# Kernel optimization log

Hardware: AMD Instinct MI355X
Metric: run time of the kernel (lower is better)

The kernel has to match this reference:

```python
import jax, jax.numpy as jnp
import numpy as np

B, S, IN_DIM, CTX = 32, 512, 256, 128
D, H, L = 128, 4, 2
DH = D // H
HID = 512
TOTAL = 11 * D * D + 8 * D  # hypernet flat weight size per sample
EPS = 1e-5


def _layernorm(x, g, b):
    mu = jnp.mean(x, axis=-1, keepdims=True)
    var = jnp.mean(jnp.square(x - mu), axis=-1, keepdims=True)
    return (x - mu) * jax.lax.rsqrt(var + EPS) * g + b


def setup_inputs() -> dict:
    key = jax.random.key(0)
    ks = jax.random.split(key, 24)
    f32 = jnp.float32
    inp = {
        'x': jax.random.normal(ks[0], (B, S, IN_DIM), f32),
        'context_vector': jax.random.normal(ks[1], (B, CTX), f32),
        'in_proj_w': jax.random.normal(ks[2], (D, IN_DIM), f32) * (IN_DIM ** -0.5),
        'in_proj_b': jnp.zeros((D,), f32),
        'pe': jax.random.normal(ks[3], (1, S, D), f32) * 0.02,
        'hfc1_w': jax.random.normal(ks[4], (L, HID, CTX), f32) * (CTX ** -0.5),
        'hfc1_b': jnp.zeros((L, HID), f32),
        'hfc2_w': jax.random.normal(ks[5], (L, TOTAL, HID), f32) * 0.02,
        'hfc2_b': jnp.zeros((L, TOTAL), f32),
        'out_proj_w': jax.random.normal(ks[6], (L, D, D), f32) * (D ** -0.5),
        'out_proj_b': jnp.zeros((L, D), f32),
        'ln1_g': jnp.ones((L, D), f32), 'ln1_b': jnp.zeros((L, D), f32),
        'ln2_g': jnp.ones((L, D), f32), 'ln2_b': jnp.zeros((L, D), f32),
        'alpha1': jnp.full((L,), 0.5, f32), 'alpha2': jnp.full((L,), 0.5, f32),
        'head_w': jax.random.normal(ks[7], (1, D), f32) * (D ** -0.5),
        'head_b': jnp.zeros((1,), f32),
    }
    return inp


def reference(x, context_vector, in_proj_w, in_proj_b, pe, hfc1_w, hfc1_b,
              hfc2_w, hfc2_b, out_proj_w, out_proj_b, ln1_g, ln1_b,
              ln2_g, ln2_b, alpha1, alpha2, head_w, head_b):
    # input projection + learned positional encoding
    h = jnp.einsum('bsi,di->bsd', x, in_proj_w) + in_proj_b
    h = h + pe[:, :h.shape[1], :]

    # flat split offsets for hypernet output
    sizes = [3 * D * D, 3 * D, 4 * D * D, 4 * D, 4 * D * D, D]
    offs = np.concatenate([[0], np.cumsum(sizes)])

    for l in range(L):
        # hypernet: per-sample weights from context
        hid = jax.nn.relu(context_vector @ hfc1_w[l].T + hfc1_b[l])
        flat = hid @ hfc2_w[l].T + hfc2_b[l]  # [B, TOTAL]
        aw = flat[:, offs[0]:offs[1]].reshape(B, 3 * D, D)
        ab = flat[:, offs[1]:offs[2]]                     # [B, 3D]
        f1w = flat[:, offs[2]:offs[3]].reshape(B, 4 * D, D)
        f1b = flat[:, offs[3]:offs[4]]                    # [B, 4D]
        f2w = flat[:, offs[4]:offs[5]].reshape(B, D, 4 * D)
        f2b = flat[:, offs[5]:offs[6]]                    # [B, D]

        # per-sample QKV projection (grouped GEMM over batch)
        qkv = jnp.einsum('bsd,bed->bse', h, aw) + ab[:, None, :]
        q, k, v = jnp.split(qkv, 3, axis=-1)
        q = q.reshape(B, S, H, DH)
        k = k.reshape(B, S, H, DH)
        v = v.reshape(B, S, H, DH)
        scores = jnp.einsum('bqhd,bkhd->bhqk', q, k) / jnp.sqrt(jnp.float32(DH))
        attn = jax.nn.softmax(scores, axis=-1)
        ctx = jnp.einsum('bhqk,bkhd->bqhd', attn, v).reshape(B, S, D)
        attn_out = jnp.einsum('bsd,ed->bse', ctx, out_proj_w[l]) + out_proj_b[l]

        h = _layernorm(h + alpha1[l] * attn_out, ln1_g[l], ln1_b[l])

        # per-sample FFN
        ff = jax.nn.relu(jnp.einsum('bsd,bfd->bsf', h, f1w) + f1b[:, None, :])
        ff = jnp.einsum('bsf,bdf->bsd', ff, f2w) + f2b[:, None, :]

        h = _layernorm(h + alpha2[l] * ff, ln2_g[l], ln2_b[l])

    out = h[:, -1, :] @ head_w.T + head_b  # [B, 1]
    return out
```

## Files before the change

### kernel.cpp

```cpp
#include <hip/hip_runtime.h>
#include <hip/hip_bf16.h>

constexpr int B_    = 32;
constexpr int S_    = 512;
constexpr int INDIM = 256;
constexpr int KCTX  = 128;
constexpr int D_    = 128;
constexpr int H_    = 4;
constexpr int L_    = 2;
constexpr int HID_  = 512;
constexpr int TOTAL_ = 11 * D_ * D_ + 8 * D_;
constexpr int OFF_AB  = 3 * D_ * D_;
constexpr int OFF_F1W = OFF_AB + 3 * D_;
constexpr int OFF_F1B = OFF_F1W + 4 * D_ * D_;
constexpr int OFF_F2W = OFF_F1B + 4 * D_;
constexpr int OFF_F2B = OFF_F2W + 4 * D_ * D_;
constexpr int TP = 132;

typedef __attribute__((ext_vector_type(8))) short short8;
typedef __attribute__((ext_vector_type(4))) short short4v;
typedef __attribute__((ext_vector_type(2))) short short2v;
typedef __attribute__((ext_vector_type(4))) float f32x4;

#define MFMA16 __builtin_amdgcn_mfma_f32_16x16x32_bf16

__device__ __forceinline__ short f2bf(float f) {
  __hip_bfloat16 h = __float2bfloat16(f);
  return __builtin_bit_cast(short, h);
}
__device__ __forceinline__ float bf2f(short s) {
  __hip_bfloat16 h = __builtin_bit_cast(__hip_bfloat16, s);
  return __bfloat162float(h);
}
struct bfpair { short hi, lo; };
__device__ __forceinline__ bfpair split2p(float x) {
  bfpair p;
  p.hi = f2bf(x);
  p.lo = f2bf(x - bf2f(p.hi));
  return p;
}

__device__ __forceinline__ long ftaddr(int row, int k, int K) {
  return ((long)(row >> 4) * (K >> 3) + (k >> 3)) * 128 + (row & 15) * 8 + (k & 7);
}

__global__ void k_cvtft(const float* __restrict__ in, short* __restrict__ oh,
                        short* __restrict__ ol, int ktShift, int n8) {
  int t = blockIdx.x * 256 + threadIdx.x;
  if (t >= n8) return;
  int kt = 1 << ktShift;
  int row = t >> ktShift;
  int kc = t & (kt - 1);
  const float* p = in + ((long)row << (ktShift + 3)) + kc * 8;
  float4 v0 = *(const float4*)p;
  float4 v1 = *(const float4*)(p + 4);
  short8 h8, l8;
  bfpair q;
  q = split2p(v0.x); h8[0] = q.hi; l8[0] = q.lo;
  q = split2p(v0.y); h8[1] = q.hi; l8[1] = q.lo;
  q = split2p(v0.z); h8[2] = q.hi; l8[2] = q.lo;
  q = split2p(v0.w); h8[3] = q.hi; l8[3] = q.lo;
  q = split2p(v1.x); h8[4] = q.hi; l8[4] = q.lo;
  q = split2p(v1.y); h8[5] = q.hi; l8[5] = q.lo;
  q = split2p(v1.z); h8[6] = q.hi; l8[6] = q.lo;
  q = split2p(v1.w); h8[7] = q.hi; l8[7] = q.lo;
  long o = ((long)(row >> 4) * kt + kc) * 128 + (row & 15) * 8;
  *(short8*)(oh + o) = h8;
  *(short8*)(ol + o) = l8;
}

__global__ __launch_bounds__(512) void k_hid(const float* __restrict__ cvec,
                                             const float* __restrict__ w,
                                             const float* __restrict__ bias,
                                             short* __restrict__ hh,
                                             short* __restrict__ hl) {
  int lb = blockIdx.x;
  int b  = lb & 31;
  int j  = threadIdx.x;
  __shared__ float cs[KCTX];
  if (j < KCTX) cs[j] = cvec[b * KCTX + j];
  __syncthreads();
  int l = lb >> 5;
  const float* wr = w + (long)(l * HID_ + j) * KCTX;
  float s = bias[l * HID_ + j];
  #pragma unroll
  for (int c = 0; c < KCTX; c += 4) {
    float4 cv = *(const float4*)(cs + c);
    float4 wv = *(const float4*)(wr + c);
    s += cv.x * wv.x + cv.y * wv.y + cv.z * wv.z + cv.w * wv.w;
  }
  s = fmaxf(s, 0.f);
  bfpair p = split2p(s);
  long o = (long)l * 32 * HID_ + ((long)(b >> 4) * 64 + (j >> 3)) * 128 + (b & 15) * 8 + (j & 7);
  hh[o] = p.hi;
  hl[o] = p.lo;
}

__global__ __launch_bounds__(256) void k_flat(
    const short* __restrict__ hidh, const short* __restrict__ hidl,
    const float* __restrict__ W, const float* __restrict__ bias,
    short* __restrict__ awh, short* __restrict__ awl,
    short* __restrict__ f1h, short* __restrict__ f1l,
    short* __restrict__ f2h, short* __restrict__ f2l,
    float* __restrict__ ab, float* __restrict__ f1b, float* __restrict__ f2b) {
  __shared__ short wls[2][64 * 64];
  const int l = blockIdx.y;
  hidh += (long)l * 32 * HID_;
  hidl += (long)l * 32 * HID_;
  W    += (long)l * TOTAL_ * HID_;
  bias += (long)l * TOTAL_;
  awh  += (long)l * B_ * 49152;  awl += (long)l * B_ * 49152;
  f1h  += (long)l * B_ * 65536;  f1l += (long)l * B_ * 65536;
  f2h  += (long)l * B_ * 65536;  f2l += (long)l * B_ * 65536;
  ab   += l * B_ * 384;  f1b += l * B_ * 512;  f2b += l * B_ * 128;
  const int tid = threadIdx.x, wave = tid >> 6, lane = tid & 63;
  const int r = lane & 15, g = lane >> 4;
  const int nb0 = blockIdx.x * 64;
  const int rr = tid >> 4;
  const int cc = (tid & 15) * 4;
  const float* wbase = W + (long)nb0 * HID_;
  float4 wv[2][4];
  #pragma unroll
  for (int rnd = 0; rnd < 4; ++rnd) {
    wv[0][rnd] = *(const float4*)(wbase + (long)(rnd * 16 + rr) * HID_ + cc);
    wv[1][rnd] = *(const float4*)(wbase + (long)(rnd * 16 + rr) * HID_ + 64 + cc);
  }
  const short* pAh = hidh + g * 128 + r * 8;
  const short* pAl = hidl + g * 128 + r * 8;
  f32x4 acc0 = {0, 0, 0, 0}, acc1 = {0, 0, 0, 0};
  int cur = 0;
  for (int c0 = 0; c0 < 512; c0 += 64) {
    #pragma unroll
    for (int rnd = 0; rnd < 4; ++rnd) {
      int row = rnd * 16 + rr;
      short4v h4, l4; bfpair q;
      q = split2p(wv[cur][rnd].x); h4[0] = q.hi; l4[0] = q.lo;
      q = split2p(wv[cur][rnd].y); h4[1] = q.hi; l4[1] = q.lo;
      q = split2p(wv[cur][rnd].z); h4[2] = q.hi; l4[2] = q.lo;
      q = split2p(wv[cur][rnd].w); h4[3] = q.hi; l4[3] = q.lo;
      int sb = row * 128 + ((cc * 2) ^ ((row & 7) << 4));
      *(short4v*)((char*)&wls[0][0] + sb) = h4;
      *(short4v*)((char*)&wls[1][0] + sb) = l4;
    }
    if (c0 + 128 < 512) {
      #pragma unroll
      for (int rnd = 0; rnd < 4; ++rnd)
        wv[cur][rnd] = *(const float4*)(wbase + (long)(rnd * 16 + rr) * HID_ + (c0 + 128) + cc);
    }
    __syncthreads();
    #pragma unroll
    for (int kk = 0; kk < 2; ++kk) {
      long ao = (long)(c0 * 16) + kk * 512;
      short8 ah0 = *(const short8*)(pAh + ao);
      short8 ah1 = *(const short8*)(pAh + 8192 + ao);
      short8 al0 = *(const short8*)(pAl + ao);
      short8 al1 = *(const short8*)(pAl + 8192 + ao);
      int wrow = wave * 16 + r;
      int wb = wrow * 128 + ((kk * 64 + g * 16) ^ ((r & 7) << 4));
      short8 wh = *(const short8*)((char*)&wls[0][0] + wb);
      short8 wl = *(const short8*)((char*)&wls[1][0] + wb);
      acc0 = MFMA16(ah0, wl, acc0, 0, 0, 0);
      acc0 = MFMA16(al0, wh, acc0, 0, 0, 0);
      acc0 = MFMA16(ah0, wh, acc0, 0, 0, 0);
      acc1 = MFMA16(ah1, wl, acc1, 0, 0, 0);
      acc1 = MFMA16(al1, wh, acc1, 0, 0, 0);
      acc1 = MFMA16(ah1, wh, acc1, 0, 0, 0);
    }
    __syncthreads();
    cur ^= 1;
  }
  constexpr int TPF = 68;
  float* tile = (float*)&wls[0][0];
  {
    int trow = nb0 + wave * 16 + r;
    float bv = bias[trow];
    int col = wave * 16 + r;
    #pragma unroll
    for (int reg = 0; reg < 4; ++reg) {
      tile[(g * 4 + reg) * TPF + col]        = acc0[reg] + bv;
      tile[(g * 4 + reg + 16) * TPF + col]   = acc1[reg] + bv;
    }
  }
  __syncthreads();
  {
    int b  = tid >> 3;
    int cg = tid & 7;
    int t0 = nb0 + cg * 8;
    float v[8];
    #pragma unroll
    for (int j = 0; j < 8; ++j) v[j] = tile[b * TPF + cg * 8 + j];
    if (t0 < OFF_AB) {
      int e = t0 >> 7, d = t0 & 127;
      long a = (long)b * 49152 + ((long)(e >> 4) * 16 + (d >> 3)) * 128 + (e & 15) * 8;
      short8 h8, l8; bfpair q;
      #pragma unroll
      for (int j = 0; j < 8; ++j) { q = split2p(v[j]); h8[j] = q.hi; l8[j] = q.lo; }
      *(short8*)(awh + a) = h8;
      *(short8*)(awl + a) = l8;
    } else if (t0 < OFF_F1W) {
      float* dst = ab + b * 384 + (t0 - OFF_AB);
      float4 x0 = {v[0], v[1], v[2], v[3]}, x1 = {v[4], v[5], v[6], v[7]};
      *(float4*)dst = x0; *(float4*)(dst + 4) = x1;
    } else if (t0 < OFF_F1B) {
      int i = t0 - OFF_F1W; int f = i >> 7, d = i & 127;
      long a = (long)b * 65536 + ((long)(f >> 4) * 16 + (d >> 3)) * 128 + (f & 15) * 8;
      short8 h8, l8; bfpair q;
      #pragma unroll
      for (int j = 0; j < 8; ++j) { q = split2p(v[j]); h8[j] = q.hi; l8[j] = q.lo; }
      *(short8*)(f1h + a) = h8;
      *(short8*)(f1l + a) = l8;
    } else if (t0 < OFF_F2W) {
      float* dst = f1b + b * 512 + (t0 - OFF_F1B);
      float4 x0 = {v[0], v[1], v[2], v[3]}, x1 = {v[4], v[5], v[6], v[7]};
      *(float4*)dst = x0; *(float4*)(dst + 4) = x1;
    } else if (t0 < OFF_F2B) {
      int i = t0 - OFF_F2W; int dd = i >> 9, f = i & 511;
      long a = (long)b * 65536 + ((long)(dd >> 4) * 64 + (f >> 3)) * 128 + (dd & 15) * 8;
      short8 h8, l8; bfpair q;
      #pragma unroll
      for (int j = 0; j < 8; ++j) { q = split2p(v[j]); h8[j] = q.hi; l8[j] = q.lo; }
      *(short8*)(f2h + a) = h8;
      *(short8*)(f2l + a) = l8;
    } else {
      float* dst = f2b + b * 128 + (t0 - OFF_F2B);
      float4 x0 = {v[0], v[1], v[2], v[3]}, x1 = {v[4], v[5], v[6], v[7]};
      *(float4*)dst = x0; *(float4*)(dst + 4) = x1;
    }
  }
}

template <int K, int EPI, bool RELU>
__global__ __launch_bounds__(256) void k_gemm(
    const short* __restrict__ Ah, const short* __restrict__ Al, long sA,
    const short* __restrict__ Wh, const short* __restrict__ Wl, long sW,
    const float* __restrict__ biasP, long sB,
    void* __restrict__ p0, void* __restrict__ p1,
    void* __restrict__ p2, void* __restrict__ p3,
    const float* __restrict__ pe, int N,
    const float* __restrict__ lng, const float* __restrict__ lnb,
    const float* __restrict__ lnal, int mOff, int nOff) {
  extern __shared__ char smem_dyn[];
  const int tid = threadIdx.x, wave = tid >> 6, lane = tid & 63;
  const int r = lane & 15, g = lane >> 4;
  const int b = blockIdx.z;
  const int bx = blockIdx.x + mOff, by = blockIdx.y + nOff;
  const int m0 = bx * 64 + (wave & 1) * 32;
  const int n0 = by * 128 + (wave >> 1) * 64;
  const long KT = (long)K * 16;
  const short* pAh = Ah + (long)b * sA + (m0 >> 4) * KT + g * 128 + r * 8;
  const short* pAl = Al + (long)b * sA + (m0 >> 4) * KT + g * 128 + r * 8;
  const short* pWh = Wh + (long)b * sW + (n0 >> 4) * KT + g * 128 + r * 8;
  const short* pWl = Wl + (long)b * sW + (n0 >> 4) * KT + g * 128 + r * 8;
  f32x4 acc[2][4] = {{{0,0,0,0},{0,0,0,0},{0,0,0,0},{0,0,0,0}},
                     {{0,0,0,0},{0,0,0,0},{0,0,0,0},{0,0,0,0}}};
  for (int kk = 0; kk < K / 32; ++kk) {
    long ko = (long)kk * 512;
    short8 a0h = *(const short8*)(pAh + ko);
    short8 a1h = *(const short8*)(pAh + KT + ko);
    short8 a0l = *(const short8*)(pAl + ko);
    short8 a1l = *(const short8*)(pAl + KT + ko);
    #pragma unroll
    for (int ns = 0; ns < 4; ++ns) {
      short8 wh = *(const short8*)(pWh + ns * KT + ko);
      short8 wl = *(const short8*)(pWl + ns * KT + ko);
      acc[0][ns] = MFMA16(a0h, wl, acc[0][ns], 0, 0, 0);
      acc[0][ns] = MFMA16(a0l, wh, acc[0][ns], 0, 0, 0);
      acc[0][ns] = MFMA16(a0h, wh, acc[0][ns], 0, 0, 0);
      acc[1][ns] = MFMA16(a1h, wl, acc[1][ns], 0, 0, 0);
      acc[1][ns] = MFMA16(a1l, wh, acc[1][ns], 0, 0, 0);
      acc[1][ns] = MFMA16(a1h, wh, acc[1][ns], 0, 0, 0);
    }
  }

  if constexpr (EPI == 5) {
    if (by == 2) {
      #pragma unroll
      for (int ms = 0; ms < 2; ++ms) {
        int crow0 = m0 + ms * 16 + g * 4;
        #pragma unroll
        for (int ns = 0; ns < 4; ++ns) {
          int ccol = n0 + ns * 16 + r;
          float bv = biasP[(long)b * sB + ccol];
          int c2 = ccol - 256, hd = c2 >> 5, dd = c2 & 31;
          short4v h4, l4; bfpair q;
          #pragma unroll
          for (int reg = 0; reg < 4; ++reg) {
            float v = acc[ms][ns][reg] + bv;
            q = split2p(v); h4[reg] = q.hi; l4[reg] = q.lo;
          }
          long o = (long)(b * 4 + hd) * 16384 + (dd >> 4) * 8192
                 + (crow0 >> 3) * 128 + (dd & 15) * 8 + (crow0 & 7);
          *(short4v*)((short*)p2 + o) = h4;
          *(short4v*)((short*)p3 + o) = l4;
        }
      }
      return;
    }
  }

  if constexpr (EPI == 1) {
    #pragma unroll
    for (int ms = 0; ms < 2; ++ms) {
      #pragma unroll
      for (int ns = 0; ns < 4; ++ns) {
        int ccol = n0 + ns * 16 + r;
        float bv = biasP[ccol];
        #pragma unroll
        for (int reg = 0; reg < 4; ++reg) {
          int crow = m0 + ms * 16 + g * 4 + reg;
          float v = acc[ms][ns][reg] + bv + pe[crow * D_ + ccol];
          ((float*)p0)[((long)b * S_ + crow) * D_ + ccol] = v;
          long o = (long)b * 65536 + (long)(crow >> 4) * 2048
                 + (ccol >> 3) * 128 + (crow & 15) * 8 + (ccol & 7);
          bfpair sp = split2p(v);
          ((short*)p1)[o] = sp.hi;
          ((short*)p2)[o] = sp.lo;
        }
      }
    }
    return;
  }

  float* tile = (float*)smem_dyn;
  #pragma unroll
  for (int ms = 0; ms < 2; ++ms) {
    #pragma unroll
    for (int ns = 0; ns < 4; ++ns) {
      int ccol = n0 + ns * 16 + r;
      float bv = biasP[(long)b * sB + ccol];
      #pragma unroll
      for (int reg = 0; reg < 4; ++reg) {
        float v = acc[ms][ns][reg] + bv;
        if constexpr (RELU) v = fmaxf(v, 0.f);
        int trow2 = (wave & 1) * 32 + ms * 16 + g * 4 + reg;
        int tcol = (wave >> 1) * 64 + ns * 16 + r;
        tile[trow2 * TP + tcol] = v;
      }
    }
  }
  __syncthreads();

  if constexpr (EPI == 0 || EPI == 5) {
    int row = tid >> 2, cg = tid & 3;
    int crow = bx * 64 + row;
    long rowbase = (long)b * 512 * N + (long)(crow >> 4) * (16 * (long)N) + (crow & 15) * 8;
    #pragma unroll
    for (int j4 = 0; j4 < 4; ++j4) {
      int tcol = j4 * 32 + cg * 8;
      float4 aa = *(const float4*)&tile[row * TP + tcol];
      float4 bb = *(const float4*)&tile[row * TP + tcol + 4];
      short8 h8, l8; bfpair q;
      q = split2p(aa.x); h8[0] = q.hi; l8[0] = q.lo;
      q = split2p(aa.y); h8[1] = q.hi; l8[1] = q.lo;
      q = split2p(aa.z); h8[2] = q.hi; l8[2] = q.lo;
      q = split2p(aa.w); h8[3] = q.hi; l8[3] = q.lo;
      q = split2p(bb.x); h8[4] = q.hi; l8[4] = q.lo;
      q = split2p(bb.y); h8[5] = q.hi; l8[5] = q.lo;
      q = split2p(bb.z); h8[6] = q.hi; l8[6] = q.lo;
      q = split2p(bb.w); h8[7] = q.hi; l8[7] = q.lo;
      int ccol = by * 128 + tcol;
      long o = rowbase + (long)(ccol >> 3) * 128;
      *(short8*)((short*)p0 + o) = h8;
      *(short8*)((short*)p1 + o) = l8;
    }
  } else if constexpr (EPI == 4) {
    int row = tid >> 2, q = tid & 3;
    int brow = bx * 64 + row;
    float a = lnal[0];
    float* hf = (float*)p0;
    float* hrow = hf + ((long)b * S_ + brow) * D_ + q * 32;
    float tv[32];
    float s = 0.f, ss = 0.f;
    #pragma unroll
    for (int i = 0; i < 32; i += 4) {
      float4 hv = *(const float4*)(hrow + i);
      float4 yv = *(const float4*)&tile[row * TP + q * 32 + i];
      float t0 = hv.x + a * yv.x, t1 = hv.y + a * yv.y;
      float t2 = hv.z + a * yv.z, t3 = hv.w + a * yv.w;
      tv[i] = t0; tv[i+1] = t1; tv[i+2] = t2; tv[i+3] = t3;
      s += t0 + t1 + t2 + t3;
      ss += t0*t0 + t1*t1 + t2*t2 + t3*t3;
    }
    s  += __shfl_xor(s, 1);  s  += __shfl_xor(s, 2);
    ss += __shfl_xor(ss, 1); ss += __shfl_xor(ss, 2);
    float mu = s * (1.f / 128.f);
    float varv = ss * (1.f / 128.f) - mu * mu;
    float inv = rsqrtf(varv + 1e-5f);
    short* ph = (short*)p1; short* pl = (short*)p2;
    long fb = (long)b * 65536 + (long)(brow >> 4) * 2048 + (brow & 15) * 8;
    #pragma unroll
    for (int j = 0; j < 4; ++j) {
      short8 hv8, lv8;
      #pragma unroll
      for (int e = 0; e < 8; e += 4) {
        int i = j * 8 + e;
        int c = q * 32 + i;
        float4 gv = *(const float4*)(lng + c);
        float4 bb = *(const float4*)(lnb + c);
        float4 o4;
        o4.x = (tv[i]   - mu) * inv * gv.x + bb.x;
        o4.y = (tv[i+1] - mu) * inv * gv.y + bb.y;
        o4.z = (tv[i+2] - mu) * inv * gv.z + bb.z;
        o4.w = (tv[i+3] - mu) * inv * gv.w + bb.w;
        *(float4*)(hrow + i) = o4;
        bfpair q0 = split2p(o4.x); hv8[e]   = q0.hi; lv8[e]   = q0.lo;
        bfpair q1 = split2p(o4.y); hv8[e+1] = q1.hi; lv8[e+1] = q1.lo;
        bfpair q2 = split2p(o4.z); hv8[e+2] = q2.hi; lv8[e+2] = q2.lo;
        bfpair q3 = split2p(o4.w); hv8[e+3] = q3.hi; lv8[e+3] = q3.lo;
      }
      long o = fb + (q * 4 + j) * 128;
      *(short8*)(ph + o) = hv8;
      *(short8*)(pl + o) = lv8;
    }
  }
}

__global__ __launch_bounds__(128) void k_attn(const short* __restrict__ qkh,
                                              const short* __restrict__ qkl,
                                              const short* __restrict__ vth,
                                              const short* __restrict__ vtl,
                                              short* __restrict__ ch,
                                              short* __restrict__ cl,
                                              int mOff) {
  __shared__ __align__(16) float scr[16][516];
  __shared__ __align__(16) float obuf[16][34];
  const int tid = threadIdx.x, wave = tid >> 6, lane = tid & 63;
  const int r = lane & 15, g = lane >> 4;
  const int b = blockIdx.z, hh = blockIdx.y;
  const int m0 = (blockIdx.x + mOff) * 16;
  const long qb = (long)b * 131072;
  const long qoff = qb + (long)(m0 >> 4) * 4096 + (hh * 4 + g) * 128 + r * 8;
  short8 qh = *(const short8*)(qkh + qoff);
  short8 ql = *(const short8*)(qkl + qoff);
  const float sc = 0.17677669529663687f;
  for (int n0 = wave * 256; n0 < wave * 256 + 256; n0 += 16) {
    long koff = qb + (long)(n0 >> 4) * 4096 + (16 + hh * 4 + g) * 128 + r * 8;
    short8 kh = *(const short8*)(qkh + koff);
    short8 kl = *(const short8*)(qkl + koff);
    f32x4 s = {0, 0, 0, 0};
    s = MFMA16(qh, kl, s, 0, 0, 0);
    s = MFMA16(ql, kh, s, 0, 0, 0);
    s = MFMA16(qh, kh, s, 0, 0, 0);
    #pragma unroll
    for (int reg = 0; reg < 4; ++reg)
      scr[g * 4 + reg][n0 + r] = s[reg] * sc;
  }
  __syncthreads();
  for (int row = wave * 8; row < wave * 8 + 8; ++row) {
    float v[8];
    #pragma unroll
    for (int i = 0; i < 8; ++i) v[i] = scr[row][lane + i * 64];
    float m = v[0];
    #pragma unroll
    for (int i = 1; i < 8; ++i) m = fmaxf(m, v[i]);
    #pragma unroll
    for (int o = 32; o > 0; o >>= 1) m = fmaxf(m, __shfl_xor(m, o));
    float ssum = 0.f;
    #pragma unroll
    for (int i = 0; i < 8; ++i) { v[i] = __expf(v[i] - m); ssum += v[i]; }
    #pragma unroll
    for (int o = 32; o > 0; o >>= 1) ssum += __shfl_xor(ssum, o);
    float inv = 1.f / ssum;
    #pragma unroll
    for (int i = 0; i < 8; ++i) scr[row][lane + i * 64] = v[i] * inv;
  }
  __syncthreads();
  f32x4 o0 = {0, 0, 0, 0}, o1 = {0, 0, 0, 0};
  const long vb = (long)(b * 4 + hh) * 16384;
  for (int kt = wave * 8; kt < wave * 8 + 8; ++kt) {
    float4 pv0 = *(const float4*)&scr[r][kt * 32 + g * 8];
    float4 pv1 = *(const float4*)&scr[r][kt * 32 + g * 8 + 4];
    short8 pah, pal;
    bfpair p;
    p = split2p(pv0.x); pah[0] = p.hi; pal[0] = p.lo;
    p = split2p(pv0.y); pah[1] = p.hi; pal[1] = p.lo;
    p = split2p(pv0.z); pah[2] = p.hi; pal[2] = p.lo;
    p = split2p(pv0.w); pah[3] = p.hi; pal[3] = p.lo;
    p = split2p(pv1.x); pah[4] = p.hi; pal[4] = p.lo;
    p = split2p(pv1.y); pah[5] = p.hi; pal[5] = p.lo;
    p = split2p(pv1.z); pah[6] = p.hi; pal[6] = p.lo;
    p = split2p(pv1.w); pah[7] = p.hi; pal[7] = p.lo;
    long vo = vb + (long)(kt * 4 + g) * 128 + r * 8;
    short8 vh0 = *(const short8*)(vth + vo);
    short8 vh1 = *(const short8*)(vth + vo + 8192);
    short8 vl0 = *(const short8*)(vtl + vo);
    short8 vl1 = *(const short8*)(vtl + vo + 8192);
    o0 = MFMA16(pah, vl0, o0, 0, 0, 0);
    o0 = MFMA16(pal, vh0, o0, 0, 0, 0);
    o0 = MFMA16(pah, vh0, o0, 0, 0, 0);
    o1 = MFMA16(pah, vl1, o1, 0, 0, 0);
    o1 = MFMA16(pal, vh1, o1, 0, 0, 0);
    o1 = MFMA16(pah, vh1, o1, 0, 0, 0);
  }
  if (wave == 1) {
    #pragma unroll
    for (int reg = 0; reg < 4; ++reg) {
      obuf[g * 4 + reg][r] = o0[reg];
      obuf[g * 4 + reg][17 + r] = o1[reg];
    }
  }
  __syncthreads();
  if (wave == 0) {
    #pragma unroll
    for (int reg = 0; reg < 4; ++reg) {
      float a0 = o0[reg] + obuf[g * 4 + reg][r];
      float a1 = o1[reg] + obuf[g * 4 + reg][17 + r];
      int srow = m0 + g * 4 + reg;
      int col0 = hh * 32 + r;
      long o = (long)b * 65536 + (long)(srow >> 4) * 2048
             + (col0 >> 3) * 128 + (srow & 15) * 8 + (col0 & 7);
      bfpair sp0 = split2p(a0);
      ch[o] = sp0.hi; cl[o] = sp0.lo;
      long o2 = o + 2 * 128;
      bfpair sp1 = split2p(a1);
      ch[o2] = sp1.hi; cl[o2] = sp1.lo;
    }
  }
}

__global__ __launch_bounds__(64) void k_head(const float* __restrict__ h,
                                             const float* __restrict__ hw,
                                             const float* __restrict__ hb,
                                             float* __restrict__ out) {
  int b = blockIdx.x, lane = threadIdx.x;
  const float* hr = h + ((long)b * S_ + (S_ - 1)) * D_;
  float v = hr[lane] * hw[lane] + hr[lane + 64] * hw[lane + 64];
  #pragma unroll
  for (int o = 32; o > 0; o >>= 1) v += __shfl_xor(v, o);
  if (lane == 0) out[b] = v + hb[0];
}

extern "C" void kernel_launch(void* const* d_in, const int* in_sizes, int n_in,
                              void* d_out, int out_size, void* d_ws, size_t ws_size,
                              hipStream_t stream) {
  const float* x    = (const float*)d_in[0];
  const float* cvec = (const float*)d_in[1];
  const float* ipw  = (const float*)d_in[2];
  const float* ipb  = (const float*)d_in[3];
  const float* pe   = (const float*)d_in[4];
  const float* h1w  = (const float*)d_in[5];
  const float* h1b  = (const float*)d_in[6];
  const float* h2w  = (const float*)d_in[7];
  const float* h2b  = (const float*)d_in[8];
  const float* opw  = (const float*)d_in[9];
  const float* opb  = (const float*)d_in[10];
  const float* ln1g = (const float*)d_in[11];
  const float* ln1b = (const float*)d_in[12];
  const float* ln2g = (const float*)d_in[13];
  const float* ln2b = (const float*)d_in[14];
  const float* a1   = (const float*)d_in[15];
  const float* a2   = (const float*)d_in[16];
  const float* hw   = (const float*)d_in[17];
  const float* hb   = (const float*)d_in[18];
  float* out = (float*)d_out;

  char* ws = (char*)d_ws;
  size_t off = 0;
  auto alloc = [&](size_t n) { void* p = ws + off; off = (off + n + 255) & ~(size_t)255; return p; };

  const long AWs = (long)B_ * 49152;
  const long F1s = (long)B_ * 65536;
  const long F2s = (long)B_ * 65536;

  short* ff1h  = (short*)alloc((size_t)B_ * S_ * 512 * 2);
  short* ff1l  = (short*)alloc((size_t)B_ * S_ * 512 * 2);
  short* xFh   = ff1h;
  short* xFl   = ff1l;
  float* h_f   = (float*)alloc((size_t)B_ * S_ * D_ * 4);
  short* hFh   = (short*)alloc((size_t)B_ * S_ * D_ * 2);
  short* hFl   = (short*)alloc((size_t)B_ * S_ * D_ * 2);
  short* hidFh = (short*)alloc((size_t)L_ * 32 * HID_ * 2);
  short* hidFl = (short*)alloc((size_t)L_ * 32 * HID_ * 2);
  short* awFh  = (short*)alloc((size_t)L_ * AWs * 2);
  short* awFl  = (short*)alloc((size_t)L_ * AWs * 2);
  short* f1wFh = (short*)alloc((size_t)L_ * F1s * 2);
  short* f1wFl = (short*)alloc((size_t)L_ * F1s * 2);
  short* f2wFh = (short*)alloc((size_t)L_ * F2s * 2);
  short* f2wFl = (short*)alloc((size_t)L_ * F2s * 2);
  float* abF   = (float*)alloc((size_t)L_ * B_ * 384 * 4);
  float* f1bF  = (float*)alloc((size_t)L_ * B_ * 512 * 4);
  float* f2bF  = (float*)alloc((size_t)L_ * B_ * 128 * 4);
  short* qkFh  = (short*)alloc((size_t)B_ * S_ * 256 * 2);
  short* qkFl  = (short*)alloc((size_t)B_ * S_ * 256 * 2);
  short* vtFh  = (short*)alloc((size_t)B_ * H_ * 32 * S_ * 2);
  short* vtFl  = (short*)alloc((size_t)B_ * H_ * 32 * S_ * 2);
  short* cxFh  = (short*)alloc((size_t)B_ * S_ * D_ * 2);
  short* cxFl  = (short*)alloc((size_t)B_ * S_ * D_ * 2);
  short* ipwFh = (short*)alloc((size_t)D_ * INDIM * 2);
  short* ipwFl = (short*)alloc((size_t)D_ * INDIM * 2);
  short* opwFh = (short*)alloc((size_t)L_ * D_ * D_ * 2);
  short* opwFl = (short*)alloc((size_t)L_ * D_ * D_ * 2);

  k_cvtft<<<(B_ * S_ * INDIM / 8 + 255) / 256, 256, 0, stream>>>(x, xFh, xFl, 5, B_ * S_ * INDIM / 8);
  k_cvtft<<<16, 256, 0, stream>>>(ipw, ipwFh, ipwFl, 5, D_ * INDIM / 8);
  k_cvtft<<<16, 256, 0, stream>>>(opw, opwFh, opwFl, 4, L_ * D_ * D_ / 8);

  k_hid<<<L_ * 32, 512, 0, stream>>>(cvec, h1w, h1b, hidFh, hidFl);

  k_flat<<<dim3(TOTAL_ / 64, 2), 256, 0, stream>>>(
      hidFh, hidFl, h2w, h2b, awFh, awFl, f1wFh, f1wFl, f2wFh, f2wFl,
      abF, f1bF, f2bF);

  k_gemm<INDIM, 1, false><<<dim3(8, 1, B_), 256, 0, stream>>>(
      xFh, xFl, (long)S_ * INDIM, ipwFh, ipwFl, 0, ipb, 0,
      h_f, hFh, hFl, nullptr, pe, 128, nullptr, nullptr, nullptr, 0, 0);

  constexpr size_t TILE_LDS = 64 * TP * 4;

  {
    int l = 0;
    k_gemm<D_, 5, false><<<dim3(8, 3, B_), 256, TILE_LDS, stream>>>(
        hFh, hFl, (long)S_ * D_, awFh + l * AWs, awFl + l * AWs, 49152,
        abF + l * B_ * 384, 384,
        qkFh, qkFl, vtFh, vtFl, nullptr, 256, nullptr, nullptr, nullptr, 0, 0);
    k_attn<<<dim3(S_ / 16, H_, B_), 128, 0, stream>>>(qkFh, qkFl, vtFh, vtFl, cxFh, cxFl, 0);
    k_gemm<D_, 4, false><<<dim3(8, 1, B_), 256, TILE_LDS, stream>>>(
        cxFh, cxFl, (long)S_ * D_, opwFh + l * 16384, opwFl + l * 16384, 0,
        opb + l * D_, 0, h_f, hFh, hFl, nullptr, nullptr, 128,
        ln1g + l * D_, ln1b + l * D_, a1 + l, 0, 0);
    k_gemm<D_, 0, true><<<dim3(8, 4, B_), 256, TILE_LDS, stream>>>(
        hFh, hFl, (long)S_ * D_, f1wFh + l * F1s, f1wFl + l * F1s, 65536,
        f1bF + l * B_ * 512, 512,
        ff1h, ff1l, nullptr, nullptr, nullptr, 512, nullptr, nullptr, nullptr, 0, 0);
    k_gemm<512, 4, false><<<dim3(8, 1, B_), 256, TILE_LDS, stream>>>(
        ff1h, ff1l, (long)S_ * 512, f2wFh + l * F2s, f2wFl + l * F2s, 65536,
        f2bF + l * B_ * 128, 128,
        h_f, hFh, hFl, nullptr, nullptr, 128,
        ln2g + l * D_, ln2b + l * D_, a2 + l, 0, 0);
  }

  {
    int l = 1;
    k_gemm<D_, 5, false><<<dim3(8, 2, B_), 256, TILE_LDS, stream>>>(
        hFh, hFl, (long)S_ * D_, awFh + l * AWs, awFl + l * AWs, 49152,
        abF + l * B_ * 384, 384,
        qkFh, qkFl, vtFh, vtFl, nullptr, 256, nullptr, nullptr, nullptr, 0, 1);
    k_gemm<D_, 5, false><<<dim3(1, 1, B_), 256, TILE_LDS, stream>>>(
        hFh, hFl, (long)S_ * D_, awFh + l * AWs, awFl + l * AWs, 49152,
        abF + l * B_ * 384, 384,
        qkFh, qkFl, vtFh, vtFl, nullptr, 256, nullptr, nullptr, nullptr, 7, 0);
    k_attn<<<dim3(1, H_, B_), 128, 0, stream>>>(qkFh, qkFl, vtFh, vtFl, cxFh, cxFl, 31);
    k_gemm<D_, 4, false><<<dim3(1, 1, B_), 256, TILE_LDS, stream>>>(
        cxFh, cxFl, (long)S_ * D_, opwFh + l * 16384, opwFl + l * 16384, 0,
        opb + l * D_, 0, h_f, hFh, hFl, nullptr, nullptr, 128,
        ln1g + l * D_, ln1b + l * D_, a1 + l, 7, 0);
    k_gemm<D_, 0, true><<<dim3(1, 4, B_), 256, TILE_LDS, stream>>>(
        hFh, hFl, (long)S_ * D_, f1wFh + l * F1s, f1wFl + l * F1s, 65536,
        f1bF + l * B_ * 512, 512,
        ff1h, ff1l, nullptr, nullptr, nullptr, 512, nullptr, nullptr, nullptr, 7, 0);
    k_gemm<512, 4, false><<<dim3(1, 1, B_), 256, TILE_LDS, stream>>>(
        ff1h, ff1l, (long)S_ * 512, f2wFh + l * F2s, f2wFl + l * F2s, 65536,
        f2bF + l * B_ * 128, 128,
        h_f, hFh, hFl, nullptr, nullptr, 128,
        ln2g + l * D_, ln2b + l * D_, a2 + l, 7, 0);
  }
  k_head<<<B_, 64, 0, stream>>>(h_f, hw, hb, out);
}
```

Measured before the change: 448.3 us.

## Merge prep kernels, co-schedule input projection with hypernet GEMM, fuse layer-1 QKV launches

Three conversion kernels and the hypernet hidden-layer kernel are folded into one launch that dispatches on block id. The input projection GEMM now runs as extra blocks inside the hypernet flat-weight kernel, so the two independent GEMMs share one launch and fill the GPU together. The two layer-1 QKV launches are merged into one grid through a block remapping mode. The aim is fewer launches and less idle time in small grids, at the cost of more branching and possible register or LDS pressure in the combined kernels.

New measurement: 440.2 us. Within noise of the previous version (-1.8%).

```diff
diff --git a/kernel.cpp b/kernel.cpp
--- a/kernel.cpp
+++ b/kernel.cpp
@@ -40,13 +40,10 @@
   return p;
 }
 
-__device__ __forceinline__ long ftaddr(int row, int k, int K) {
-  return ((long)(row >> 4) * (K >> 3) + (k >> 3)) * 128 + (row & 15) * 8 + (k & 7);
-}
-
-__global__ void k_cvtft(const float* __restrict__ in, short* __restrict__ oh,
-                        short* __restrict__ ol, int ktShift, int n8) {
-  int t = blockIdx.x * 256 + threadIdx.x;
+__device__ __forceinline__ void cvt_body(const float* __restrict__ in,
+                                         short* __restrict__ oh,
+                                         short* __restrict__ ol,
+                                         int ktShift, int n8, int t) {
   if (t >= n8) return;
   int kt = 1 << ktShift;
   int row = t >> ktShift;
@@ -54,8 +51,7 @@
   const float* p = in + ((long)row << (ktShift + 3)) + kc * 8;
   float4 v0 = *(const float4*)p;
   float4 v1 = *(const float4*)(p + 4);
-  short8 h8, l8;
-  bfpair q;
+  short8 h8, l8; bfpair q;
   q = split2p(v0.x); h8[0] = q.hi; l8[0] = q.lo;
   q = split2p(v0.y); h8[1] = q.hi; l8[1] = q.lo;
   q = split2p(v0.z); h8[2] = q.hi; l8[2] = q.lo;
@@ -69,42 +65,125 @@
   *(short8*)(ol + o) = l8;
 }
 
-__global__ __launch_bounds__(512) void k_hid(const float* __restrict__ cvec,
-                                             const float* __restrict__ w,
-                                             const float* __restrict__ bias,
-                                             short* __restrict__ hh,
-                                             short* __restrict__ hl) {
-  int lb = blockIdx.x;
-  int b  = lb & 31;
-  int j  = threadIdx.x;
-  __shared__ float cs[KCTX];
-  if (j < KCTX) cs[j] = cvec[b * KCTX + j];
-  __syncthreads();
-  int l = lb >> 5;
-  const float* wr = w + (long)(l * HID_ + j) * KCTX;
-  float s = bias[l * HID_ + j];
+__global__ __launch_bounds__(256) void k_prep(
+    const float* __restrict__ x, const float* __restrict__ ipw,
+    const float* __restrict__ opw,
+    short* __restrict__ xFh, short* __restrict__ xFl,
+    short* __restrict__ ipwFh, short* __restrict__ ipwFl,
+    short* __restrict__ opwFh, short* __restrict__ opwFl,
+    const float* __restrict__ cvec, const float* __restrict__ h1w,
+    const float* __restrict__ h1b,
+    short* __restrict__ hidFh, short* __restrict__ hidFl) {
+  int id = blockIdx.x, tid = threadIdx.x;
+  if (id < 2048) {
+    cvt_body(x, xFh, xFl, 5, B_ * S_ * INDIM / 8, id * 256 + tid);
+  } else if (id < 2064) {
+    cvt_body(ipw, ipwFh, ipwFl, 5, D_ * INDIM / 8, (id - 2048) * 256 + tid);
+  } else if (id < 2080) {
+    cvt_body(opw, opwFh, opwFl, 4, L_ * D_ * D_ / 8, (id - 2064) * 256 + tid);
+  } else {
+    int hb = id - 2080;
+    int l = hb >> 5, b = hb & 31;
+    __shared__ float cs[KCTX];
+    if (tid < KCTX) cs[tid] = cvec[b * KCTX + tid];
+    __syncthreads();
+    #pragma unroll
+    for (int jj = 0; jj < 2; ++jj) {
+      int j = tid + jj * 256;
+      const float* wr = h1w + (long)(l * HID_ + j) * KCTX;
+      float s = h1b[l * HID_ + j];
+      #pragma unroll
+      for (int c = 0; c < KCTX; c += 4) {
+        float4 cv = *(const float4*)(cs + c);
+        float4 wv = *(const float4*)(wr + c);
+        s += cv.x * wv.x + cv.y * wv.y + cv.z * wv.z + cv.w * wv.w;
+      }
+      s = fmaxf(s, 0.f);
+      bfpair p = split2p(s);
+      long o = (long)l * 32 * HID_ + ((long)(b >> 4) * 64 + (j >> 3)) * 128
+             + (b & 15) * 8 + (j & 7);
+      hidFh[o] = p.hi;
+      hidFl[o] = p.lo;
+    }
+  }
+}
+
+__device__ void inproj_block(int id,
+    const short* __restrict__ xFh, const short* __restrict__ xFl,
+    const short* __restrict__ ipwFh, const short* __restrict__ ipwFl,
+    const float* __restrict__ ipb, const float* __restrict__ pe,
+    float* __restrict__ h_f, short* __restrict__ hFh, short* __restrict__ hFl) {
+  const int tid = threadIdx.x, wave = tid >> 6, lane = tid & 63;
+  const int r = lane & 15, g = lane >> 4;
+  const int bx = id >> 5, b = id & 31;
+  const int m0 = bx * 64 + (wave & 1) * 32;
+  const int n0 = (wave >> 1) * 64;
+  const long KT = (long)INDIM * 16;
+  const short* pAh = xFh + (long)b * S_ * INDIM + (m0 >> 4) * KT + g * 128 + r * 8;
+  const short* pAl = xFl + (long)b * S_ * INDIM + (m0 >> 4) * KT + g * 128 + r * 8;
+  const short* pWh = ipwFh + (n0 >> 4) * KT + g * 128 + r * 8;
+  const short* pWl = ipwFl + (n0 >> 4) * KT + g * 128 + r * 8;
+  f32x4 acc[2][4] = {{{0,0,0,0},{0,0,0,0},{0,0,0,0},{0,0,0,0}},
+                     {{0,0,0,0},{0,0,0,0},{0,0,0,0},{0,0,0,0}}};
+  for (int kk = 0; kk < INDIM / 32; ++kk) {
+    long ko = (long)kk * 512;
+    short8 a0h = *(const short8*)(pAh + ko);
+    short8 a1h = *(const short8*)(pAh + KT + ko);
+    short8 a0l = *(const short8*)(pAl + ko);
+    short8 a1l = *(const short8*)(pAl + KT + ko);
+    #pragma unroll
+    for (int ns = 0; ns < 4; ++ns) {
+      short8 wh = *(const short8*)(pWh + ns * KT + ko);
+      short8 wl = *(const short8*)(pWl + ns * KT + ko);
+      acc[0][ns] = MFMA16(a0h, wl, acc[0][ns], 0, 0, 0);
+      acc[0][ns] = MFMA16(a0l, wh, acc[0][ns], 0, 0, 0);
+      acc[0][ns] = MFMA16(a0h, wh, acc[0][ns], 0, 0, 0);
+      acc[1][ns] = MFMA16(a1h, wl, acc[1][ns], 0, 0, 0);
+      acc[1][ns] = MFMA16(a1l, wh, acc[1][ns], 0, 0, 0);
+      acc[1][ns] = MFMA16(a1h, wh, acc[1][ns], 0, 0, 0);
+    }
+  }
   #pragma unroll
-  for (int c = 0; c < KCTX; c += 4) {
-    float4 cv = *(const float4*)(cs + c);
-    float4 wv = *(const float4*)(wr + c);
-    s += cv.x * wv.x + cv.y * wv.y + cv.z * wv.z + cv.w * wv.w;
-  }
-  s = fmaxf(s, 0.f);
-  bfpair p = split2p(s);
-  long o = (long)l * 32 * HID_ + ((long)(b >> 4) * 64 + (j >> 3)) * 128 + (b & 15) * 8 + (j & 7);
-  hh[o] = p.hi;
-  hl[o] = p.lo;
-}
-
-__global__ __launch_bounds__(256) void k_flat(
+  for (int ms = 0; ms < 2; ++ms) {
+    #pragma unroll
+    for (int ns = 0; ns < 4; ++ns) {
+      int ccol = n0 + ns * 16 + r;
+      float bv = ipb[ccol];
+      #pragma unroll
+      for (int reg = 0; reg < 4; ++reg) {
+        int crow = m0 + ms * 16 + g * 4 + reg;
+        float v = acc[ms][ns][reg] + bv + pe[crow * D_ + ccol];
+        h_f[((long)b * S_ + crow) * D_ + ccol] = v;
+        long o = (long)b * 65536 + (long)(crow >> 4) * 2048
+               + (ccol >> 3) * 128 + (crow & 15) * 8 + (ccol & 7);
+        bfpair sp = split2p(v);
+        hFh[o] = sp.hi;
+        hFl[o] = sp.lo;
+      }
+    }
+  }
+}
+
+__global__ __launch_bounds__(256) void k_flat_ip(
     const short* __restrict__ hidh, const short* __restrict__ hidl,
     const float* __restrict__ W, const float* __restrict__ bias,
     short* __restrict__ awh, short* __restrict__ awl,
     short* __restrict__ f1h, short* __restrict__ f1l,
     short* __restrict__ f2h, short* __restrict__ f2l,
-    float* __restrict__ ab, float* __restrict__ f1b, float* __restrict__ f2b) {
+    float* __restrict__ ab, float* __restrict__ f1b, float* __restrict__ f2b,
+    const short* __restrict__ xFh, const short* __restrict__ xFl,
+    const short* __restrict__ ipwFh, const short* __restrict__ ipwFl,
+    const float* __restrict__ ipb, const float* __restrict__ pe,
+    float* __restrict__ h_f, short* __restrict__ hFh, short* __restrict__ hFl) {
   __shared__ short wls[2][64 * 64];
-  const int l = blockIdx.y;
+  const int id = blockIdx.x;
+  if (id < 256) {
+    inproj_block(id, xFh, xFl, ipwFh, ipwFl, ipb, pe, h_f, hFh, hFl);
+    return;
+  }
+  const int fid = id - 256;
+  const int l = fid / 2832;
+  const int bxf = fid % 2832;
   hidh += (long)l * 32 * HID_;
   hidl += (long)l * 32 * HID_;
   W    += (long)l * TOTAL_ * HID_;
@@ -115,7 +194,7 @@
   ab   += l * B_ * 384;  f1b += l * B_ * 512;  f2b += l * B_ * 128;
   const int tid = threadIdx.x, wave = tid >> 6, lane = tid & 63;
   const int r = lane & 15, g = lane >> 4;
-  const int nb0 = blockIdx.x * 64;
+  const int nb0 = bxf * 64;
   const int rr = tid >> 4;
   const int cc = (tid & 15) * 4;
   const float* wbase = W + (long)nb0 * HID_;
@@ -172,13 +251,12 @@
   constexpr int TPF = 68;
   float* tile = (float*)&wls[0][0];
   {
-    int trow = nb0 + wave * 16 + r;
-    float bv = bias[trow];
+    float bv = bias[nb0 + wave * 16 + r];
     int col = wave * 16 + r;
     #pragma unroll
     for (int reg = 0; reg < 4; ++reg) {
-      tile[(g * 4 + reg) * TPF + col]        = acc0[reg] + bv;
-      tile[(g * 4 + reg + 16) * TPF + col]   = acc1[reg] + bv;
+      tile[(g * 4 + reg) * TPF + col]      = acc0[reg] + bv;
+      tile[(g * 4 + reg + 16) * TPF + col] = acc1[reg] + bv;
     }
   }
   __syncthreads();
@@ -236,14 +314,21 @@
     const float* __restrict__ biasP, long sB,
     void* __restrict__ p0, void* __restrict__ p1,
     void* __restrict__ p2, void* __restrict__ p3,
-    const float* __restrict__ pe, int N,
+    int N,
     const float* __restrict__ lng, const float* __restrict__ lnb,
-    const float* __restrict__ lnal, int mOff, int nOff) {
+    const float* __restrict__ lnal, int mOff, int nOff, int mode) {
   extern __shared__ char smem_dyn[];
   const int tid = threadIdx.x, wave = tid >> 6, lane = tid & 63;
   const int r = lane & 15, g = lane >> 4;
   const int b = blockIdx.z;
-  const int bx = blockIdx.x + mOff, by = blockIdx.y + nOff;
+  int bx, by;
+  if (mode == 1) {
+    int xx = blockIdx.x;
+    if (xx < 16) { bx = xx >> 1; by = 1 + (xx & 1); }
+    else         { bx = 7; by = 0; }
+  } else {
+    bx = blockIdx.x + mOff; by = blockIdx.y + nOff;
+  }
   const int m0 = bx * 64 + (wave & 1) * 32;
   const int n0 = by * 128 + (wave >> 1) * 64;
   const long KT = (long)K * 16;
@@ -296,29 +381,6 @@
       }
       return;
     }
-  }
-
-  if constexpr (EPI == 1) {
-    #pragma unroll
-    for (int ms = 0; ms < 2; ++ms) {
-      #pragma unroll
-      for (int ns = 0; ns < 4; ++ns) {
-        int ccol = n0 + ns * 16 + r;
-        float bv = biasP[ccol];
-        #pragma unroll
-        for (int reg = 0; reg < 4; ++reg) {
-          int crow = m0 + ms * 16 + g * 4 + reg;
-          float v = acc[ms][ns][reg] + bv + pe[crow * D_ + ccol];
-          ((float*)p0)[((long)b * S_ + crow) * D_ + ccol] = v;
-          long o = (long)b * 65536 + (long)(crow >> 4) * 2048
-                 + (ccol >> 3) * 128 + (crow & 15) * 8 + (ccol & 7);
-          bfpair sp = split2p(v);
-          ((short*)p1)[o] = sp.hi;
-          ((short*)p2)[o] = sp.lo;
-        }
-      }
-    }
-    return;
   }
 
   float* tile = (float*)smem_dyn;
@@ -591,19 +653,13 @@
   short* opwFh = (short*)alloc((size_t)L_ * D_ * D_ * 2);
   short* opwFl = (short*)alloc((size_t)L_ * D_ * D_ * 2);
 
-  k_cvtft<<<(B_ * S_ * INDIM / 8 + 255) / 256, 256, 0, stream>>>(x, xFh, xFl, 5, B_ * S_ * INDIM / 8);
-  k_cvtft<<<16, 256, 0, stream>>>(ipw, ipwFh, ipwFl, 5, D_ * INDIM / 8);
-  k_cvtft<<<16, 256, 0, stream>>>(opw, opwFh, opwFl, 4, L_ * D_ * D_ / 8);
-
-  k_hid<<<L_ * 32, 512, 0, stream>>>(cvec, h1w, h1b, hidFh, hidFl);
-
-  k_flat<<<dim3(TOTAL_ / 64, 2), 256, 0, stream>>>(
+  k_prep<<<2144, 256, 0, stream>>>(x, ipw, opw, xFh, xFl, ipwFh, ipwFl,
+                                   opwFh, opwFl, cvec, h1w, h1b, hidFh, hidFl);
+
+  k_flat_ip<<<256 + 2 * 2832, 256, 0, stream>>>(
       hidFh, hidFl, h2w, h2b, awFh, awFl, f1wFh, f1wFl, f2wFh, f2wFl,
-      abF, f1bF, f2bF);
-
-  k_gemm<INDIM, 1, false><<<dim3(8, 1, B_), 256, 0, stream>>>(
-      xFh, xFl, (long)S_ * INDIM, ipwFh, ipwFl, 0, ipb, 0,
-      h_f, hFh, hFl, nullptr, pe, 128, nullptr, nullptr, nullptr, 0, 0);
+      abF, f1bF, f2bF,
+      xFh, xFl, ipwFh, ipwFl, ipb, pe, h_f, hFh, hFl);
 
   constexpr size_t TILE_LDS = 64 * TP * 4;
 
@@ -612,47 +668,43 @@
     k_gemm<D_, 5, false><<<dim3(8, 3, B_), 256, TILE_LDS, stream>>>(
         hFh, hFl, (long)S_ * D_, awFh + l * AWs, awFl + l * AWs, 49152,
         abF + l * B_ * 384, 384,
-        qkFh, qkFl, vtFh, vtFl, nullptr, 256, nullptr, nullptr, nullptr, 0, 0);
+        qkFh, qkFl, vtFh, vtFl, 256, nullptr, nullptr, nullptr, 0, 0, 0);
     k_attn<<<dim3(S_ / 16, H_, B_), 128, 0, stream>>>(qkFh, qkFl, vtFh, vtFl, cxFh, cxFl, 0);
     k_gemm<D_, 4, false><<<dim3(8, 1, B_), 256, TILE_LDS, stream>>>(
         cxFh, cxFl, (long)S_ * D_, opwFh + l * 16384, opwFl + l * 16384, 0,
-        opb + l * D_, 0, h_f, hFh, hFl, nullptr, nullptr, 128,
-        ln1g + l * D_, ln1b + l * D_, a1 + l, 0, 0);
+        opb + l * D_, 0, h_f, hFh, hFl, nullptr, 128,
+        ln1g + l * D_, ln1b + l * D_, a1 + l, 0, 0, 0);
     k_gemm<D_, 0, true><<<dim3(8, 4, B_), 256, TILE_LDS, stream>>>(
         hFh, hFl, (long)S_ * D_, f1wFh + l * F1s, f1wFl + l * F1s, 65536,
         f1bF + l * B_ * 512, 512,
-        ff1h, ff1l, nullptr, nullptr, nullptr, 512, nullptr, nullptr, nullptr, 0, 0);
+        ff1h, ff1l, nullptr, nullptr, 512, nullptr, nullptr, nullptr, 0, 0, 0);
     k_gemm<512, 4, false><<<dim3(8, 1, B_), 256, TILE_LDS, stream>>>(
         ff1h, ff1l, (long)S_ * 512, f2wFh + l * F2s, f2wFl + l * F2s, 65536,
         f2bF + l * B_ * 128, 128,
-        h_f, hFh, hFl, nullptr, nullptr, 128,
-        ln2g + l * D_, ln2b + l * D_, a2 + l, 0, 0);
+        h_f, hFh, hFl, nullptr, 128,
+        ln2g + l * D_, ln2b + l * D_, a2 + l, 0, 0, 0);
   }
 
   {
     int l = 1;
-    k_gemm<D_, 5, false><<<dim3(8, 2, B_), 256, TILE_LDS, stream>>>(
+    k_gemm<D_, 5, false><<<dim3(17, 1, B_), 256, TILE_LDS, stream>>>(
         hFh, hFl, (long)S_ * D_, awFh + l * AWs, awFl + l * AWs, 49152,
         abF + l * B_ * 384, 384,
-        qkFh, qkFl, vtFh, vtFl, nullptr, 256, nullptr, nullptr, nullptr, 0, 1);
-    k_gemm<D_, 5, false><<<dim3(1, 1, B_), 256, TILE_LDS, stream>>>(
-        hFh, hFl, (long)S_ * D_, awFh + l * AWs, awFl + l * AWs, 49152,
-        abF + l * B_ * 384, 384,
-        qkFh, qkFl, vtFh, vtFl, nullptr, 256, nullptr, nullptr, nullptr, 7, 0);
+        qkFh, qkFl, vtFh, vtFl, 256, nullptr, nullptr, nullptr, 0, 0, 1);
     k_attn<<<dim3(1, H_, B_), 128, 0, stream>>>(qkFh, qkFl, vtFh, vtFl, cxFh, cxFl, 31);
     k_gemm<D_, 4, false><<<dim3(1, 1, B_), 256, TILE_LDS, stream>>>(
         cxFh, cxFl, (long)S_ * D_, opwFh + l * 16384, opwFl + l * 16384, 0,
-        opb + l * D_, 0, h_f, hFh, hFl, nullptr, nullptr, 128,
-        ln1g + l * D_, ln1b + l * D_, a1 + l, 7, 0);
+        opb + l * D_, 0, h_f, hFh, hFl, nullptr, 128,
+        ln1g + l * D_, ln1b + l * D_, a1 + l, 7, 0, 0);
     k_gemm<D_, 0, true><<<dim3(1, 4, B_), 256, TILE_LDS, stream>>>(
         hFh, hFl, (long)S_ * D_, f1wFh + l * F1s, f1wFl + l * F1s, 65536,
         f1bF + l * B_ * 512, 512,
-        ff1h, ff1l, nullptr, nullptr, nullptr, 512, nullptr, nullptr, nullptr, 7, 0);
+        ff1h, ff1l, nullptr, nullptr, 512, nullptr, nullptr, nullptr, 7, 0, 0);
     k_gemm<512, 4, false><<<dim3(1, 1, B_), 256, TILE_LDS, stream>>>(
         ff1h, ff1l, (long)S_ * 512, f2wFh + l * F2s, f2wFl + l * F2s, 65536,
         f2bF + l * B_ * 128, 128,
-        h_f, hFh, hFl, nullptr, nullptr, 128,
-        ln2g + l * D_, ln2b + l * D_, a2 + l, 7, 0);
+        h_f, hFh, hFl, nullptr, 128,
+        ln2g + l * D_, ln2b + l * D_, a2 + l, 7, 0, 0);
   }
   k_head<<<B_, 64, 0, stream>>>(h_f, hw, hb, out);
 }
```
